# Performance work log

Measured on AMD Instinct MI355X. Metric: run time of the kernel, lower is better.

## Reference

```python
import jax, jax.numpy as jnp
import numpy as np

N_HEAD, D_MODEL, D_K, D_V = 16, 1024, 64, 64
BN_EPS = 1e-5
NEG_INF = -1e9


def setup_inputs() -> dict:
    key = jax.random.key(0)
    ks = jax.random.split(key, 10)
    B, L = 4, 1024
    q = jax.random.normal(ks[0], (B, L, D_MODEL), dtype=jnp.float32)
    k = jax.random.normal(ks[1], (B, L, D_MODEL), dtype=jnp.float32)
    v = jax.random.normal(ks[2], (B, L, D_MODEL), dtype=jnp.float32)
    attn_mask = jax.random.randint(ks[3], (B, L, L), 0, 2) == 1  # True -> masked out
    s = 1.0 / np.sqrt(D_MODEL)
    w_qs = jax.random.normal(ks[4], (N_HEAD, D_MODEL, D_K), dtype=jnp.float32) * s
    w_ks = jax.random.normal(ks[5], (N_HEAD, D_MODEL, D_K), dtype=jnp.float32) * s
    w_vs = jax.random.normal(ks[6], (N_HEAD, D_MODEL, D_V), dtype=jnp.float32) * s
    proj_w = jax.random.normal(ks[7], (D_MODEL, N_HEAD * D_V), dtype=jnp.float32) * s
    proj_b = jnp.zeros((D_MODEL,), dtype=jnp.float32)
    bn_gamma = jnp.ones((D_MODEL,), dtype=jnp.float32)
    bn_beta = jnp.zeros((D_MODEL,), dtype=jnp.float32)
    return {"q": q, "k": k, "v": v, "attn_mask": attn_mask,
            "w_qs": w_qs, "w_ks": w_ks, "w_vs": w_vs,
            "proj_w": proj_w, "proj_b": proj_b,
            "bn_gamma": bn_gamma, "bn_beta": bn_beta}


def reference(q, k, v, attn_mask, w_qs, w_ks, w_vs, proj_w, proj_b, bn_gamma, bn_beta):
    B, Lq, D = q.shape
    temper = jnp.asarray(np.sqrt(D), dtype=q.dtype)
    residual = q
    # per-head projections: (H, B, L, dk)
    qh = jnp.einsum('bld,hdk->hblk', q, w_qs)
    kh = jnp.einsum('bld,hdk->hblk', k, w_ks)
    vh = jnp.einsum('bld,hdv->hblv', v, w_vs)
    # scaled dot-product attention, temper = sqrt(d_model)
    scores = jnp.einsum('hbqk,hbsk->hbqs', qh, kh) / temper
    scores = jnp.where(attn_mask[None], NEG_INF, scores)
    attns = jax.nn.softmax(scores, axis=-1)  # (H, B, Lq, Lk)
    out_h = jnp.einsum('hbqs,hbsv->hbqv', attns, vh)  # (H, B, Lq, dv)
    # concat heads along feature dim in head order
    out = jnp.transpose(out_h, (1, 2, 0, 3)).reshape(B, Lq, N_HEAD * D_V)
    out = out @ proj_w.T + proj_b
    # residual + BatchNorm1d over channel dim (batch stats, training-mode math)
    x = out + residual  # (B, L, D)
    mean = jnp.mean(x, axis=(0, 1))
    var = jnp.var(x, axis=(0, 1))
    x = (x - mean) * jax.lax.rsqrt(var + BN_EPS) * bn_gamma + bn_beta
    attns_flat = attns.reshape(N_HEAD * B, Lq, -1)
    return x, attns_flat
```

## Files before the change

### kernel.cpp

```cpp
#include <hip/hip_runtime.h>

typedef unsigned short ushort;
typedef __attribute__((ext_vector_type(4))) float floatx4;
typedef __bf16 bf16x8 __attribute__((ext_vector_type(8)));
typedef __bf16 bf16x4 __attribute__((ext_vector_type(4)));
typedef float f32x4 __attribute__((ext_vector_type(4)));

constexpr int NB = 4;
constexpr int NL = 1024;
constexpr int ND = 1024;
constexpr int NH = 16;
constexpr int NDK = 64;

union B4 { bf16x4 v; unsigned long long ll; };

__device__ __forceinline__ void st_bf(ushort* dst, float f){
  union { __bf16 h; ushort u; } z; z.h = (__bf16)f; *dst = z.u;
}

#define MFMA(a,b,c) __builtin_amdgcn_mfma_f32_16x16x32_bf16((a),(b),(c),0,0,0)

__global__ __launch_bounds__(256) void k_prep(const float* __restrict__ q,
                                              const float* __restrict__ k,
                                              const float* __restrict__ v,
                                              const float* __restrict__ pw,
                                              const float* __restrict__ w0,
                                              const float* __restrict__ w1,
                                              const float* __restrict__ w2,
                                              const int* __restrict__ M,
                                              ushort* __restrict__ qb,
                                              ushort* __restrict__ kb,
                                              ushort* __restrict__ vb,
                                              ushort* __restrict__ pwb,
                                              ushort* __restrict__ t0,
                                              ushort* __restrict__ t1,
                                              ushort* __restrict__ t2,
                                              unsigned long long* __restrict__ MB,
                                              float* __restrict__ part){
  __shared__ ushort T[64][65];
  const int bid = blockIdx.x;
  const int tid = threadIdx.x;

  if (bid < 6656){
    const int a = (bid < 2048) ? 0 : (bid < 4096) ? 1 : (bid < 6144) ? 2 : 3;
    const int rel = bid - a * 2048;
    const float* src = (a == 0) ? q : (a == 1) ? k : (a == 2) ? v : pw;
    ushort* dst = (a == 0) ? qb : (a == 1) ? kb : (a == 2) ? vb : pwb;
    const size_t base = ((size_t)rel * 256 + tid) * 8;
    floatx4 v0 = *(const floatx4*)(src + base);
    floatx4 v1 = *(const floatx4*)(src + base + 4);
    bf16x8 o;
    #pragma unroll
    for (int j = 0; j < 4; j++){ o[j] = (__bf16)v0[j]; o[4 + j] = (__bf16)v1[j]; }
    *(bf16x8*)(dst + base) = o;
    return;
  }
  if (bid < 7424){
    const int r = bid - 6656;
    const int z = r >> 8;
    const int h = (r >> 4) & 15, k0 = (r & 15) * 64;
    const float* src = (z == 0) ? w0 : (z == 1) ? w1 : w2;
    ushort* dst = (z == 0) ? t0 : (z == 1) ? t1 : t2;
    const int qd = tid >> 6, lo = tid & 63;
    #pragma unroll
    for (int i = 0; i < 16; i++){
      int kl = qd + i * 4;
      float f = src[((size_t)h * 1024 + k0 + kl) * 64 + lo];
      union { __bf16 h2; ushort u; } zz; zz.h2 = (__bf16)f;
      T[kl][lo] = zz.u;
    }
    __syncthreads();
    #pragma unroll
    for (int i = 0; i < 16; i++){
      int dk = qd + i * 4;
      dst[((size_t)h * 64 + dk) * 1024 + k0 + lo] = T[lo][dk];
    }
    return;
  }
  if (bid < 11520){
    const int r = bid - 7424;
    #pragma unroll
    for (int rep = 0; rep < 4; rep++){
      const int gid = r * 1024 + rep * 256 + tid;
      const int widx = gid >> 6;
      int m = M[(size_t)widx * 64 + (gid & 63)];
      unsigned long long bal = __ballot(m != 0);
      if ((gid & 63) == 0) MB[widx] = bal;
    }
    return;
  }
  *(floatx4*)(part + tid * 8) = f32x4{0.f, 0.f, 0.f, 0.f};
  *(floatx4*)(part + tid * 8 + 4) = f32x4{0.f, 0.f, 0.f, 0.f};
}

__global__ __launch_bounds__(256) void k_projm(const ushort* __restrict__ qbp,
                                               const ushort* __restrict__ kbp,
                                               const ushort* __restrict__ vbp,
                                               const ushort* __restrict__ wqT,
                                               const ushort* __restrict__ wkT,
                                               const ushort* __restrict__ wvT,
                                               ushort* __restrict__ qh,
                                               ushort* __restrict__ kh,
                                               ushort* __restrict__ vt){
  __shared__ bf16x8 Ach[8 * 128];
  __shared__ bf16x8 Bch[8 * 128];
  const int z = blockIdx.z;
  const ushort* Xb = (z == 0) ? qbp : (z == 1) ? kbp : vbp;
  const ushort* WT = (z == 0) ? wqT : (z == 1) ? wkT : wvT;
  const int tid = threadIdx.x;
  const int lane = tid & 63, wid = tid >> 6;
  const int g = lane >> 4, c = lane & 15;
  const int d = blockIdx.y * 8 + blockIdx.x;
  const int tile = (d & 7) * 32 + (d >> 3);
  const int row0 = (tile >> 3) * 128, col0 = (tile & 7) * 128;
  const int wm = (wid >> 1) * 64, wn = (wid & 1) * 64;

  f32x4 zero = {0.f, 0.f, 0.f, 0.f};
  f32x4 acc[4][4];
  #pragma unroll
  for (int i = 0; i < 4; i++)
    #pragma unroll
    for (int j = 0; j < 4; j++) acc[i][j] = zero;

  for (int k0 = 0; k0 < ND; k0 += 64){
    #pragma unroll
    for (int i = 0; i < 4; i++){
      int e = tid + i * 256;
      int kc = e & 7, m = e >> 3;
      Ach[kc * 128 + (m ^ kc)] = *(const bf16x8*)(Xb + (size_t)(row0 + m) * ND + k0 + kc * 8);
    }
    #pragma unroll
    for (int i = 0; i < 4; i++){
      int e = tid + i * 256;
      int kc = e & 7, n = e >> 3;
      int hh = (col0 + n) >> 6, dk = (col0 + n) & 63;
      Bch[kc * 128 + (n ^ kc)] = *(const bf16x8*)(WT + ((size_t)(hh << 6) + dk) * 1024 + k0 + kc * 8);
    }
    __syncthreads();
    bf16x8 bfr[4][2];
    #pragma unroll
    for (int ni = 0; ni < 4; ni++){
      int n = wn + ni * 16 + c;
      bfr[ni][0] = Bch[g * 128 + (n ^ g)];
      bfr[ni][1] = Bch[(4 + g) * 128 + (n ^ (4 + g))];
    }
    #pragma unroll
    for (int mi = 0; mi < 4; mi++){
      int m = wm + mi * 16 + c;
      bf16x8 a0 = Ach[g * 128 + (m ^ g)];
      bf16x8 a1 = Ach[(4 + g) * 128 + (m ^ (4 + g))];
      #pragma unroll
      for (int ni = 0; ni < 4; ni++){
        acc[mi][ni] = MFMA(a0, bfr[ni][0], acc[mi][ni]);
        acc[mi][ni] = MFMA(a1, bfr[ni][1], acc[mi][ni]);
      }
    }
    __syncthreads();
  }
  if (z == 2){
    #pragma unroll
    for (int mi = 0; mi < 4; mi++){
      #pragma unroll
      for (int ni = 0; ni < 4; ni++){
        int n = col0 + wn + ni * 16 + c;
        int hh = n >> 6, dk = n & 63;
        int m0 = row0 + wm + mi * 16 + g * 4;
        int bb = m0 >> 10, l = m0 & 1023;
        B4 o;
        #pragma unroll
        for (int r = 0; r < 4; r++) o.v[r] = (__bf16)acc[mi][ni][r];
        *(unsigned long long*)(vt + (((size_t)hh * NB + bb) * 64 + dk) * 1024 + l) = o.ll;
      }
    }
  } else {
    ushort* OUT = (z == 0) ? qh : kh;
    #pragma unroll
    for (int mi = 0; mi < 4; mi++){
      #pragma unroll
      for (int ni = 0; ni < 4; ni++){
        #pragma unroll
        for (int r = 0; r < 4; r++){
          int m = row0 + wm + mi * 16 + g * 4 + r;
          int n = col0 + wn + ni * 16 + c;
          int bb = m >> 10, ls = m & 1023;
          int hh = n >> 6, dk = n & 63;
          st_bf(OUT + (((size_t)hh * NB + bb) * NL + ls) * NDK + dk, acc[mi][ni][r]);
        }
      }
    }
  }
}

__global__ __launch_bounds__(256, 4) void k_attn(const ushort* __restrict__ QH,
                                                 const ushort* __restrict__ KH,
                                                 const ushort* __restrict__ VT,
                                                 const unsigned* __restrict__ MB,
                                                 float* __restrict__ ATT,
                                                 ushort* __restrict__ CTX){
  __shared__ bf16x8 Kch[512];
  __shared__ bf16x8 Vch[512];
  __shared__ ushort Ps[4][16][72];
  __shared__ unsigned Ms[64 * 33];
  const int tid = threadIdx.x;
  const int lane = tid & 63, wid = tid >> 6;
  const int g = lane >> 4, c = lane & 15;
  const int d = blockIdx.y * 16 + blockIdx.x;
  const int tile = (d & 7) * 128 + (d >> 3);
  const int hb = tile >> 4;
  const int q0 = (tile & 15) * 64;
  const int h = hb >> 2, b = hb & 3;

  const int q = q0 + wid * 16 + c;
  const size_t qkbase = (size_t)hb * NL;

  bf16x8 qf0 = *(const bf16x8*)(QH + (qkbase + q) * NDK + g * 8);
  bf16x8 qf1 = *(const bf16x8*)(QH + (qkbase + q) * NDK + 32 + g * 8);

  {
    const unsigned* mbase = MB + ((size_t)(b << 10) + q0) * 32;
    #pragma unroll
    for (int i = 0; i < 8; i++){
      int idx = tid + i * 256;
      int ql2 = idx >> 5, word = idx & 31;
      Ms[ql2 * 33 + word] = mbase[ql2 * 32 + word];
    }
  }
  const int ql = wid * 16 + c;
  const int mg = g * 4;

  float rs = 0.f;
  for (int t = 0; t < 16; ++t){
    __syncthreads();
    const ushort* ksrc = KH + (qkbase + t * 64) * NDK;
    #pragma unroll
    for (int i = 0; i < 2; i++){
      int idx = tid * 2 + i;
      int sr = idx >> 3, kc = idx & 7;
      Kch[sr * 8 + (kc ^ (sr & 7))] = *(const bf16x8*)(ksrc + idx * 8);
    }
    __syncthreads();
    #pragma unroll
    for (int sub2 = 0; sub2 < 4; ++sub2){
      int s = sub2 * 16 + c;
      bf16x8 kf0 = Kch[s * 8 + (g ^ (s & 7))];
      bf16x8 kf1 = Kch[s * 8 + ((4 + g) ^ (s & 7))];
      f32x4 a = {0.f, 0.f, 0.f, 0.f};
      a = MFMA(kf0, qf0, a);
      a = MFMA(kf1, qf1, a);
      unsigned w = Ms[ql * 33 + t * 2 + (sub2 >> 1)];
      unsigned bits4 = (w >> (((sub2 & 1) << 4) + mg)) & 0xFu;
      #pragma unroll
      for (int r = 0; r < 4; r++)
        rs += ((bits4 >> r) & 1u) ? 0.f : __expf(a[r] * (1.f / 32.f));
    }
  }
  rs += __shfl_xor(rs, 16);
  rs += __shfl_xor(rs, 32);
  const float invd = 1.f / rs;

  f32x4 zero = {0.f, 0.f, 0.f, 0.f};
  f32x4 acc[4];
  #pragma unroll
  for (int i = 0; i < 4; i++) acc[i] = zero;

  for (int t = 0; t < 16; ++t){
    __syncthreads();
    const ushort* ksrc = KH + (qkbase + t * 64) * NDK;
    #pragma unroll
    for (int i = 0; i < 2; i++){
      int idx = tid * 2 + i;
      int sr = idx >> 3, kc = idx & 7;
      Kch[sr * 8 + (kc ^ (sr & 7))] = *(const bf16x8*)(ksrc + idx * 8);
    }
    #pragma unroll
    for (int i = 0; i < 2; i++){
      int idx = tid + i * 256;
      int dv = idx >> 3, kc = idx & 7;
      Vch[kc * 64 + (dv ^ kc)] = *(const bf16x8*)(VT + ((size_t)hb * 64 + dv) * 1024 + t * 64 + kc * 8);
    }
    __syncthreads();
    #pragma unroll
    for (int sub2 = 0; sub2 < 4; ++sub2){
      int s = sub2 * 16 + c;
      bf16x8 kf0 = Kch[s * 8 + (g ^ (s & 7))];
      bf16x8 kf1 = Kch[s * 8 + ((4 + g) ^ (s & 7))];
      f32x4 a = {0.f, 0.f, 0.f, 0.f};
      a = MFMA(kf0, qf0, a);
      a = MFMA(kf1, qf1, a);
      unsigned w = Ms[ql * 33 + t * 2 + (sub2 >> 1)];
      unsigned bits4 = (w >> (((sub2 & 1) << 4) + mg)) & 0xFu;
      floatx4 pn;
      B4 pw;
      #pragma unroll
      for (int r = 0; r < 4; r++){
        float p = ((bits4 >> r) & 1u) ? 0.f : __expf(a[r] * (1.f / 32.f)) * invd;
        pn[r] = p;
        pw.v[r] = (__bf16)p;
      }
      *(floatx4*)(ATT + ((size_t)hb * NL + q) * NL + (t * 4 + sub2) * 16 + g * 4) = pn;
      *(unsigned long long*)&Ps[wid][c][sub2 * 16 + g * 4] = pw.ll;
    }
    #pragma unroll
    for (int ss = 0; ss < 2; ++ss){
      bf16x8 afr = *(bf16x8*)&Ps[wid][c][ss * 32 + g * 8];
      #pragma unroll
      for (int ni = 0; ni < 4; ni++){
        int kcr = ss * 4 + g;
        bf16x8 vfr = Vch[kcr * 64 + ((ni * 16 + c) ^ kcr)];
        acc[ni] = MFMA(afr, vfr, acc[ni]);
      }
    }
  }

  #pragma unroll
  for (int ni = 0; ni < 4; ni++)
    #pragma unroll
    for (int r = 0; r < 4; r++){
      int qq = q0 + wid * 16 + g * 4 + r;
      int dv = ni * 16 + c;
      st_bf(CTX + ((size_t)b * NL + qq) * ND + h * NDK + dv, acc[ni][r]);
    }
}

__global__ __launch_bounds__(256) void k_projo(const ushort* __restrict__ CTX,
                                               const ushort* __restrict__ PWb,
                                               const float* __restrict__ PB,
                                               const float* __restrict__ RES,
                                               float* __restrict__ X,
                                               float* __restrict__ part){
  __shared__ bf16x8 Ach[8 * 128];
  __shared__ bf16x8 Bch[8 * 128];
  const int tid = threadIdx.x;
  const int lane = tid & 63, wid = tid >> 6;
  const int g = lane >> 4, c = lane & 15;
  const int d = blockIdx.y * 8 + blockIdx.x;
  const int tile = (d & 7) * 32 + (d >> 3);
  const int row0 = (tile >> 3) * 128, col0 = (tile & 7) * 128;
  const int wm = (wid >> 1) * 64, wn = (wid & 1) * 64;

  f32x4 zero = {0.f, 0.f, 0.f, 0.f};
  f32x4 acc[4][4];
  #pragma unroll
  for (int i = 0; i < 4; i++)
    #pragma unroll
    for (int j = 0; j < 4; j++) acc[i][j] = zero;

  for (int k0 = 0; k0 < ND; k0 += 64){
    #pragma unroll
    for (int i = 0; i < 4; i++){
      int e = tid + i * 256;
      int kc = e & 7, m = e >> 3;
      Ach[kc * 128 + (m ^ kc)] = *(const bf16x8*)(CTX + (size_t)(row0 + m) * ND + k0 + kc * 8);
    }
    #pragma unroll
    for (int i = 0; i < 4; i++){
      int e = tid + i * 256;
      int kc = e & 7, n = e >> 3;
      Bch[kc * 128 + (n ^ kc)] = *(const bf16x8*)(PWb + (size_t)(col0 + n) * 1024 + k0 + kc * 8);
    }
    __syncthreads();
    bf16x8 bfr[4][2];
    #pragma unroll
    for (int ni = 0; ni < 4; ni++){
      int n = wn + ni * 16 + c;
      bfr[ni][0] = Bch[g * 128 + (n ^ g)];
      bfr[ni][1] = Bch[(4 + g) * 128 + (n ^ (4 + g))];
    }
    #pragma unroll
    for (int mi = 0; mi < 4; mi++){
      int m = wm + mi * 16 + c;
      bf16x8 a0 = Ach[g * 128 + (m ^ g)];
      bf16x8 a1 = Ach[(4 + g) * 128 + (m ^ (4 + g))];
      #pragma unroll
      for (int ni = 0; ni < 4; ni++){
        acc[mi][ni] = MFMA(a0, bfr[ni][0], acc[mi][ni]);
        acc[mi][ni] = MFMA(a1, bfr[ni][1], acc[mi][ni]);
      }
    }
    __syncthreads();
  }
  float s_[4] = {0.f, 0.f, 0.f, 0.f}, s2_[4] = {0.f, 0.f, 0.f, 0.f};
  #pragma unroll
  for (int mi = 0; mi < 4; mi++)
    #pragma unroll
    for (int ni = 0; ni < 4; ni++)
      #pragma unroll
      for (int r = 0; r < 4; r++){
        int m = row0 + wm + mi * 16 + g * 4 + r;
        int n = col0 + wn + ni * 16 + c;
        float val = acc[mi][ni][r] + PB[n] + RES[(size_t)m * ND + n];
        X[(size_t)m * ND + n] = val;
        s_[ni] += val; s2_[ni] += val * val;
      }
  #pragma unroll
  for (int ni = 0; ni < 4; ni++){
    float a = s_[ni], b2 = s2_[ni];
    a += __shfl_xor(a, 16); b2 += __shfl_xor(b2, 16);
    a += __shfl_xor(a, 32); b2 += __shfl_xor(b2, 32);
    if (g == 0){
      int n = col0 + wn + ni * 16 + c;
      atomicAdd(&part[n], a);
      atomicAdd(&part[1024 + n], b2);
    }
  }
}

__global__ __launch_bounds__(256) void k_bnst2(const float* __restrict__ part,
                                               float* __restrict__ MV){
  const int cx = blockIdx.x * 256 + threadIdx.x;
  float s = part[cx], s2 = part[1024 + cx];
  float mean = s * (1.f / (NB * NL));
  float var = s2 * (1.f / (NB * NL)) - mean * mean;
  MV[cx] = mean;
  MV[ND + cx] = rsqrtf(var + 1e-5f);
}

__global__ __launch_bounds__(256) void k_bnapply(float* __restrict__ X,
                                                 const float* __restrict__ MV,
                                                 const float* __restrict__ G,
                                                 const float* __restrict__ Bt){
  const int idx = blockIdx.x * 256 + threadIdx.x;
  const size_t base = (size_t)idx * 8;
  const int d0 = (int)(base & (ND - 1));
  floatx4 x0 = *(const floatx4*)(X + base);
  floatx4 x1 = *(const floatx4*)(X + base + 4);
  floatx4 o0, o1;
  #pragma unroll
  for (int e = 0; e < 4; e++){
    int d = d0 + e;
    o0[e] = (x0[e] - MV[d]) * MV[ND + d] * G[d] + Bt[d];
    int d2 = d0 + 4 + e;
    o1[e] = (x1[e] - MV[d2]) * MV[ND + d2] * G[d2] + Bt[d2];
  }
  *(floatx4*)(X + base) = o0;
  *(floatx4*)(X + base + 4) = o1;
}

extern "C" void kernel_launch(void* const* d_in, const int* in_sizes, int n_in,
                              void* d_out, int out_size, void* d_ws, size_t ws_size,
                              hipStream_t stream){
  const float* q      = (const float*)d_in[0];
  const float* k      = (const float*)d_in[1];
  const float* v      = (const float*)d_in[2];
  const int*   mask   = (const int*)d_in[3];
  const float* w_qs   = (const float*)d_in[4];
  const float* w_ks   = (const float*)d_in[5];
  const float* w_vs   = (const float*)d_in[6];
  const float* proj_w = (const float*)d_in[7];
  const float* proj_b = (const float*)d_in[8];
  const float* gamma  = (const float*)d_in[9];
  const float* beta   = (const float*)d_in[10];

  float* out_x   = (float*)d_out;
  float* out_att = out_x + (size_t)NB * NL * ND;

  char* ws = (char*)d_ws;
  ushort* qb  = (ushort*)(ws);
  ushort* kb  = (ushort*)(ws + (8u  << 20));
  ushort* vb  = (ushort*)(ws + (16u << 20));
  ushort* qh  = (ushort*)(ws + (24u << 20));
  ushort* kh  = (ushort*)(ws + (32u << 20));
  ushort* vt  = (ushort*)(ws + (40u << 20));
  ushort* wqT = (ushort*)(ws + (48u << 20));
  ushort* wkT = (ushort*)(ws + (50u << 20));
  ushort* wvT = (ushort*)(ws + (52u << 20));
  ushort* pwb = (ushort*)(ws + (54u << 20));
  unsigned long long* mb = (unsigned long long*)(ws + (56u << 20));
  float*  part = (float*)(ws + (57u << 20));
  float*  mv   = (float*)(ws + (58u << 20));
  ushort* ctx  = qb;

  dim3 blk(256);
  k_prep<<<dim3(11521), blk, 0, stream>>>(q, k, v, proj_w, w_qs, w_ks, w_vs, mask,
                                          qb, kb, vb, pwb, wqT, wkT, wvT, mb, part);
  k_projm<<<dim3(8, 32, 3), blk, 0, stream>>>(qb, kb, vb, wqT, wkT, wvT, qh, kh, vt);
  k_attn<<<dim3(16, 64), blk, 0, stream>>>(qh, kh, vt, (const unsigned*)mb, out_att, ctx);
  k_projo<<<dim3(8, 32), blk, 0, stream>>>(ctx, pwb, proj_b, q, out_x, part);
  k_bnst2<<<dim3(4), blk, 0, stream>>>(part, mv);
  k_bnapply<<<dim3(NB * NL * ND / 8 / 256), blk, 0, stream>>>(out_x, mv, gamma, beta);
}
```

Baseline: 195.0 us.

## Fuse fp32-to-bf16 input conversion into projection GEMM and fold BN stats kernel

The separate pass that converted q, k and v to bf16 is removed. The projection GEMM now loads fp32 directly and converts to bf16 while staging into shared memory, which avoids writing and re-reading about 24MB of bf16 intermediates. The BN statistics kernel is folded into bn-apply, so mean and rstd are recomputed per element and one launch disappears. Nontemporal stores are used for the attention-probability and final outputs, and a nontemporal load for the residual. The cost is that the GEMM reads twice as many input bytes per tile and now does conversion arithmetic in its load path.

```diff
diff --git a/kernel.cpp b/kernel.cpp
--- a/kernel.cpp
+++ b/kernel.cpp
@@ -20,17 +20,11 @@
 
 #define MFMA(a,b,c) __builtin_amdgcn_mfma_f32_16x16x32_bf16((a),(b),(c),0,0,0)
 
-__global__ __launch_bounds__(256) void k_prep(const float* __restrict__ q,
-                                              const float* __restrict__ k,
-                                              const float* __restrict__ v,
-                                              const float* __restrict__ pw,
+__global__ __launch_bounds__(256) void k_prep(const float* __restrict__ pw,
                                               const float* __restrict__ w0,
                                               const float* __restrict__ w1,
                                               const float* __restrict__ w2,
                                               const int* __restrict__ M,
-                                              ushort* __restrict__ qb,
-                                              ushort* __restrict__ kb,
-                                              ushort* __restrict__ vb,
                                               ushort* __restrict__ pwb,
                                               ushort* __restrict__ t0,
                                               ushort* __restrict__ t1,
@@ -41,22 +35,18 @@
   const int bid = blockIdx.x;
   const int tid = threadIdx.x;
 
-  if (bid < 6656){
-    const int a = (bid < 2048) ? 0 : (bid < 4096) ? 1 : (bid < 6144) ? 2 : 3;
-    const int rel = bid - a * 2048;
-    const float* src = (a == 0) ? q : (a == 1) ? k : (a == 2) ? v : pw;
-    ushort* dst = (a == 0) ? qb : (a == 1) ? kb : (a == 2) ? vb : pwb;
-    const size_t base = ((size_t)rel * 256 + tid) * 8;
-    floatx4 v0 = *(const floatx4*)(src + base);
-    floatx4 v1 = *(const floatx4*)(src + base + 4);
+  if (bid < 512){
+    const size_t base = ((size_t)bid * 256 + tid) * 8;
+    floatx4 v0 = *(const floatx4*)(pw + base);
+    floatx4 v1 = *(const floatx4*)(pw + base + 4);
     bf16x8 o;
     #pragma unroll
     for (int j = 0; j < 4; j++){ o[j] = (__bf16)v0[j]; o[4 + j] = (__bf16)v1[j]; }
-    *(bf16x8*)(dst + base) = o;
+    *(bf16x8*)(pwb + base) = o;
     return;
   }
-  if (bid < 7424){
-    const int r = bid - 6656;
+  if (bid < 1280){
+    const int r = bid - 512;
     const int z = r >> 8;
     const int h = (r >> 4) & 15, k0 = (r & 15) * 64;
     const float* src = (z == 0) ? w0 : (z == 1) ? w1 : w2;
@@ -77,8 +67,8 @@
     }
     return;
   }
-  if (bid < 11520){
-    const int r = bid - 7424;
+  if (bid < 5376){
+    const int r = bid - 1280;
     #pragma unroll
     for (int rep = 0; rep < 4; rep++){
       const int gid = r * 1024 + rep * 256 + tid;
@@ -93,9 +83,9 @@
   *(floatx4*)(part + tid * 8 + 4) = f32x4{0.f, 0.f, 0.f, 0.f};
 }
 
-__global__ __launch_bounds__(256) void k_projm(const ushort* __restrict__ qbp,
-                                               const ushort* __restrict__ kbp,
-                                               const ushort* __restrict__ vbp,
+__global__ __launch_bounds__(256) void k_projm(const float* __restrict__ qf,
+                                               const float* __restrict__ kf,
+                                               const float* __restrict__ vf,
                                                const ushort* __restrict__ wqT,
                                                const ushort* __restrict__ wkT,
                                                const ushort* __restrict__ wvT,
@@ -105,7 +95,7 @@
   __shared__ bf16x8 Ach[8 * 128];
   __shared__ bf16x8 Bch[8 * 128];
   const int z = blockIdx.z;
-  const ushort* Xb = (z == 0) ? qbp : (z == 1) ? kbp : vbp;
+  const float* Xf = (z == 0) ? qf : (z == 1) ? kf : vf;
   const ushort* WT = (z == 0) ? wqT : (z == 1) ? wkT : wvT;
   const int tid = threadIdx.x;
   const int lane = tid & 63, wid = tid >> 6;
@@ -127,7 +117,13 @@
     for (int i = 0; i < 4; i++){
       int e = tid + i * 256;
       int kc = e & 7, m = e >> 3;
-      Ach[kc * 128 + (m ^ kc)] = *(const bf16x8*)(Xb + (size_t)(row0 + m) * ND + k0 + kc * 8);
+      const float* src = Xf + (size_t)(row0 + m) * ND + k0 + kc * 8;
+      floatx4 v0 = *(const floatx4*)src;
+      floatx4 v1 = *(const floatx4*)(src + 4);
+      bf16x8 pb;
+      #pragma unroll
+      for (int j = 0; j < 4; j++){ pb[j] = (__bf16)v0[j]; pb[4 + j] = (__bf16)v1[j]; }
+      Ach[kc * 128 + (m ^ kc)] = pb;
     }
     #pragma unroll
     for (int i = 0; i < 4; i++){
@@ -297,7 +293,8 @@
         pn[r] = p;
         pw.v[r] = (__bf16)p;
       }
-      *(floatx4*)(ATT + ((size_t)hb * NL + q) * NL + (t * 4 + sub2) * 16 + g * 4) = pn;
+      __builtin_nontemporal_store(pn,
+        (floatx4*)(ATT + ((size_t)hb * NL + q) * NL + (t * 4 + sub2) * 16 + g * 4));
       *(unsigned long long*)&Ps[wid][c][sub2 * 16 + g * 4] = pw.ll;
     }
     #pragma unroll
@@ -388,7 +385,8 @@
       for (int r = 0; r < 4; r++){
         int m = row0 + wm + mi * 16 + g * 4 + r;
         int n = col0 + wn + ni * 16 + c;
-        float val = acc[mi][ni][r] + PB[n] + RES[(size_t)m * ND + n];
+        float rv = __builtin_nontemporal_load(RES + (size_t)m * ND + n);
+        float val = acc[mi][ni][r] + PB[n] + rv;
         X[(size_t)m * ND + n] = val;
         s_[ni] += val; s2_[ni] += val * val;
       }
@@ -405,18 +403,8 @@
   }
 }
 
-__global__ __launch_bounds__(256) void k_bnst2(const float* __restrict__ part,
-                                               float* __restrict__ MV){
-  const int cx = blockIdx.x * 256 + threadIdx.x;
-  float s = part[cx], s2 = part[1024 + cx];
-  float mean = s * (1.f / (NB * NL));
-  float var = s2 * (1.f / (NB * NL)) - mean * mean;
-  MV[cx] = mean;
-  MV[ND + cx] = rsqrtf(var + 1e-5f);
-}
-
 __global__ __launch_bounds__(256) void k_bnapply(float* __restrict__ X,
-                                                 const float* __restrict__ MV,
+                                                 const float* __restrict__ part,
                                                  const float* __restrict__ G,
                                                  const float* __restrict__ Bt){
   const int idx = blockIdx.x * 256 + threadIdx.x;
@@ -425,15 +413,22 @@
   floatx4 x0 = *(const floatx4*)(X + base);
   floatx4 x1 = *(const floatx4*)(X + base + 4);
   floatx4 o0, o1;
+  constexpr float invN = 1.f / (NB * NL);
   #pragma unroll
   for (int e = 0; e < 4; e++){
     int d = d0 + e;
-    o0[e] = (x0[e] - MV[d]) * MV[ND + d] * G[d] + Bt[d];
+    float mean = part[d] * invN;
+    float var = part[1024 + d] * invN - mean * mean;
+    float rstd = rsqrtf(var + 1e-5f);
+    o0[e] = (x0[e] - mean) * rstd * G[d] + Bt[d];
     int d2 = d0 + 4 + e;
-    o1[e] = (x1[e] - MV[d2]) * MV[ND + d2] * G[d2] + Bt[d2];
-  }
-  *(floatx4*)(X + base) = o0;
-  *(floatx4*)(X + base + 4) = o1;
+    float mean2 = part[d2] * invN;
+    float var2 = part[1024 + d2] * invN - mean2 * mean2;
+    float rstd2 = rsqrtf(var2 + 1e-5f);
+    o1[e] = (x1[e] - mean2) * rstd2 * G[d2] + Bt[d2];
+  }
+  __builtin_nontemporal_store(o0, (floatx4*)(X + base));
+  __builtin_nontemporal_store(o1, (floatx4*)(X + base + 4));
 }
 
 extern "C" void kernel_launch(void* const* d_in, const int* in_sizes, int n_in,
@@ -455,27 +450,23 @@
   float* out_att = out_x + (size_t)NB * NL * ND;
 
   char* ws = (char*)d_ws;
-  ushort* qb  = (ushort*)(ws);
-  ushort* kb  = (ushort*)(ws + (8u  << 20));
-  ushort* vb  = (ushort*)(ws + (16u << 20));
-  ushort* qh  = (ushort*)(ws + (24u << 20));
-  ushort* kh  = (ushort*)(ws + (32u << 20));
-  ushort* vt  = (ushort*)(ws + (40u << 20));
-  ushort* wqT = (ushort*)(ws + (48u << 20));
-  ushort* wkT = (ushort*)(ws + (50u << 20));
-  ushort* wvT = (ushort*)(ws + (52u << 20));
-  ushort* pwb = (ushort*)(ws + (54u << 20));
-  unsigned long long* mb = (unsigned long long*)(ws + (56u << 20));
-  float*  part = (float*)(ws + (57u << 20));
-  float*  mv   = (float*)(ws + (58u << 20));
-  ushort* ctx  = qb;
+  ushort* qh  = (ushort*)(ws);
+  ushort* kh  = (ushort*)(ws + (8u  << 20));
+  ushort* vt  = (ushort*)(ws + (16u << 20));
+  ushort* wqT = (ushort*)(ws + (24u << 20));
+  ushort* wkT = (ushort*)(ws + (26u << 20));
+  ushort* wvT = (ushort*)(ws + (28u << 20));
+  ushort* pwb = (ushort*)(ws + (30u << 20));
+  unsigned long long* mb = (unsigned long long*)(ws + (32u << 20));
+  float*  part = (float*)(ws + (33u << 20));
+  ushort* ctx  = qh;
+  ctx = (ushort*)(ws + (34u << 20));
 
   dim3 blk(256);
-  k_prep<<<dim3(11521), blk, 0, stream>>>(q, k, v, proj_w, w_qs, w_ks, w_vs, mask,
-                                          qb, kb, vb, pwb, wqT, wkT, wvT, mb, part);
-  k_projm<<<dim3(8, 32, 3), blk, 0, stream>>>(qb, kb, vb, wqT, wkT, wvT, qh, kh, vt);
+  k_prep<<<dim3(5377), blk, 0, stream>>>(proj_w, w_qs, w_ks, w_vs, mask,
+                                         pwb, wqT, wkT, wvT, mb, part);
+  k_projm<<<dim3(8, 32, 3), blk, 0, stream>>>(q, k, v, wqT, wkT, wvT, qh, kh, vt);
   k_attn<<<dim3(16, 64), blk, 0, stream>>>(qh, kh, vt, (const unsigned*)mb, out_att, ctx);
   k_projo<<<dim3(8, 32), blk, 0, stream>>>(ctx, pwb, proj_b, q, out_x, part);
-  k_bnst2<<<dim3(4), blk, 0, stream>>>(part, mv);
-  k_bnapply<<<dim3(NB * NL * ND / 8 / 256), blk, 0, stream>>>(out_x, mv, gamma, beta);
-}
+  k_bnapply<<<dim3(NB * NL * ND / 8 / 256), blk, 0, stream>>>(out_x, part, gamma, beta);
+}
```

Result: slower. 203.9 us (+4.6%).

## Prefetch K/V tiles into registers and fold softmax scale into Q projection

Applied to the files above, without the earlier changes.

The attention kernel now loads the next K and V tiles from global memory into registers while the current tile is being computed, so global load latency overlaps with the MFMA and exp work instead of sitting between barriers. The 1/32 temperature and log2(e) factor are folded into the bf16 Q projection output, which lets the softmax use a raw exp2 instruction without a per-element multiply. This raises register pressure under the 4-waves occupancy bound. Scaling Q before the bf16 rounding also changes rounding slightly.

```diff
diff --git a/kernel.cpp b/kernel.cpp
--- a/kernel.cpp
+++ b/kernel.cpp
@@ -11,6 +11,8 @@
 constexpr int ND = 1024;
 constexpr int NH = 16;
 constexpr int NDK = 64;
+
+#define QSCALE 0.045084230079650879f
 
 union B4 { bf16x4 v; unsigned long long ll; };
 
@@ -174,6 +176,7 @@
     }
   } else {
     ushort* OUT = (z == 0) ? qh : kh;
+    const float sc = (z == 0) ? QSCALE : 1.0f;
     #pragma unroll
     for (int mi = 0; mi < 4; mi++){
       #pragma unroll
@@ -184,7 +187,7 @@
           int n = col0 + wn + ni * 16 + c;
           int bb = m >> 10, ls = m & 1023;
           int hh = n >> 6, dk = n & 63;
-          st_bf(OUT + (((size_t)hh * NB + bb) * NL + ls) * NDK + dk, acc[mi][ni][r]);
+          st_bf(OUT + (((size_t)hh * NB + bb) * NL + ls) * NDK + dk, acc[mi][ni][r] * sc);
         }
       }
     }
@@ -228,17 +231,25 @@
   const int ql = wid * 16 + c;
   const int mg = g * 4;
 
+  const int i0 = tid * 2, i1 = tid * 2 + 1;
+  const int sr0 = i0 >> 3, kc0 = i0 & 7;
+  const int sr1 = i1 >> 3, kc1 = i1 & 7;
+  const int vdv0 = tid >> 3, vkc0 = tid & 7;
+  const int vdv1 = (tid + 256) >> 3, vkc1 = tid & 7;
+
   float rs = 0.f;
+  bf16x8 kr0 = *(const bf16x8*)(KH + (qkbase + 0) * NDK + i0 * 8);
+  bf16x8 kr1 = *(const bf16x8*)(KH + (qkbase + 0) * NDK + i1 * 8);
   for (int t = 0; t < 16; ++t){
     __syncthreads();
-    const ushort* ksrc = KH + (qkbase + t * 64) * NDK;
-    #pragma unroll
-    for (int i = 0; i < 2; i++){
-      int idx = tid * 2 + i;
-      int sr = idx >> 3, kc = idx & 7;
-      Kch[sr * 8 + (kc ^ (sr & 7))] = *(const bf16x8*)(ksrc + idx * 8);
-    }
-    __syncthreads();
+    Kch[sr0 * 8 + (kc0 ^ (sr0 & 7))] = kr0;
+    Kch[sr1 * 8 + (kc1 ^ (sr1 & 7))] = kr1;
+    __syncthreads();
+    if (t < 15){
+      const ushort* knext = KH + (qkbase + (t + 1) * 64) * NDK;
+      kr0 = *(const bf16x8*)(knext + i0 * 8);
+      kr1 = *(const bf16x8*)(knext + i1 * 8);
+    }
     #pragma unroll
     for (int sub2 = 0; sub2 < 4; ++sub2){
       int s = sub2 * 16 + c;
@@ -251,7 +262,7 @@
       unsigned bits4 = (w >> (((sub2 & 1) << 4) + mg)) & 0xFu;
       #pragma unroll
       for (int r = 0; r < 4; r++)
-        rs += ((bits4 >> r) & 1u) ? 0.f : __expf(a[r] * (1.f / 32.f));
+        rs += ((bits4 >> r) & 1u) ? 0.f : __builtin_amdgcn_exp2f(a[r]);
     }
   }
   rs += __shfl_xor(rs, 16);
@@ -263,22 +274,26 @@
   #pragma unroll
   for (int i = 0; i < 4; i++) acc[i] = zero;
 
+  kr0 = *(const bf16x8*)(KH + (qkbase + 0) * NDK + i0 * 8);
+  kr1 = *(const bf16x8*)(KH + (qkbase + 0) * NDK + i1 * 8);
+  bf16x8 vr0 = *(const bf16x8*)(VT + ((size_t)hb * 64 + vdv0) * 1024 + vkc0 * 8);
+  bf16x8 vr1 = *(const bf16x8*)(VT + ((size_t)hb * 64 + vdv1) * 1024 + vkc1 * 8);
+
   for (int t = 0; t < 16; ++t){
     __syncthreads();
-    const ushort* ksrc = KH + (qkbase + t * 64) * NDK;
-    #pragma unroll
-    for (int i = 0; i < 2; i++){
-      int idx = tid * 2 + i;
-      int sr = idx >> 3, kc = idx & 7;
-      Kch[sr * 8 + (kc ^ (sr & 7))] = *(const bf16x8*)(ksrc + idx * 8);
-    }
-    #pragma unroll
-    for (int i = 0; i < 2; i++){
-      int idx = tid + i * 256;
-      int dv = idx >> 3, kc = idx & 7;
-      Vch[kc * 64 + (dv ^ kc)] = *(const bf16x8*)(VT + ((size_t)hb * 64 + dv) * 1024 + t * 64 + kc * 8);
-    }
-    __syncthreads();
+    Kch[sr0 * 8 + (kc0 ^ (sr0 & 7))] = kr0;
+    Kch[sr1 * 8 + (kc1 ^ (sr1 & 7))] = kr1;
+    Vch[vkc0 * 64 + (vdv0 ^ vkc0)] = vr0;
+    Vch[vkc1 * 64 + (vdv1 ^ vkc1)] = vr1;
+    __syncthreads();
+    if (t < 15){
+      const ushort* knext = KH + (qkbase + (t + 1) * 64) * NDK;
+      kr0 = *(const bf16x8*)(knext + i0 * 8);
+      kr1 = *(const bf16x8*)(knext + i1 * 8);
+      const ushort* vnext = VT + (size_t)hb * 64 * 1024 + (t + 1) * 64;
+      vr0 = *(const bf16x8*)(vnext + (size_t)vdv0 * 1024 + vkc0 * 8);
+      vr1 = *(const bf16x8*)(vnext + (size_t)vdv1 * 1024 + vkc1 * 8);
+    }
     #pragma unroll
     for (int sub2 = 0; sub2 < 4; ++sub2){
       int s = sub2 * 16 + c;
@@ -293,7 +308,7 @@
       B4 pw;
       #pragma unroll
       for (int r = 0; r < 4; r++){
-        float p = ((bits4 >> r) & 1u) ? 0.f : __expf(a[r] * (1.f / 32.f)) * invd;
+        float p = ((bits4 >> r) & 1u) ? 0.f : __builtin_amdgcn_exp2f(a[r]) * invd;
         pn[r] = p;
         pw.v[r] = (__bf16)p;
       }
```

After: 187.2 us. -4.0%, faster.
